# Optimization experiments

Measured on AMD Instinct MI355X. Metric: run time of the kernel, lower is better.

The kernel has to match this reference:

```python
import jax, jax.numpy as jnp
import numpy as np

THETA = 10000.0

def _rope_cache(seq_len, d_k, dtype=jnp.float32):
    # theta_k = theta ** (-(2i/d_k)), angles[n, i] = n * theta_k[i]
    inv_freq = THETA ** (-(jnp.arange(0, d_k, 2, dtype=jnp.float32) / d_k))
    pos = jnp.arange(seq_len, dtype=jnp.float32)
    ang = pos[:, None] * inv_freq[None, :]          # [S, d_k/2]
    cos = jnp.repeat(jnp.cos(ang), 2, axis=-1)      # [S, d_k]
    sin = jnp.repeat(jnp.sin(ang), 2, axis=-1)
    return cos.astype(dtype), sin.astype(dtype)

def _apply_rope(x, cos, sin):
    # x: [..., S, d_k]; rotate even/odd pairs: rot[2i] = -x[2i+1], rot[2i+1] = x[2i]
    x2 = x.reshape(x.shape[:-1] + (x.shape[-1] // 2, 2))
    rot = jnp.stack([-x2[..., 1], x2[..., 0]], axis=-1).reshape(x.shape)
    return x * cos + rot * sin

def setup_inputs() -> dict:
    key = jax.random.key(0)
    ks = jax.random.split(key, 5)
    B, S, D = 2, 2048, 1024
    H, DK = 16, 64
    scale = (2.0 / (D + DK)) ** 0.5
    x = jax.random.normal(ks[0], (B, S, D), dtype=jnp.float32)
    Wq = jax.random.normal(ks[1], (H, D, DK), dtype=jnp.float32) * scale
    Wk = jax.random.normal(ks[2], (H, D, DK), dtype=jnp.float32) * scale
    Wv = jax.random.normal(ks[3], (H, D, DK), dtype=jnp.float32) * scale
    Wo = jax.random.normal(ks[4], (D, D), dtype=jnp.float32) * (2.0 / (2 * D)) ** 0.5
    return {"x": x, "Wq": Wq, "Wk": Wk, "Wv": Wv, "Wo": Wo}

def reference(x, Wq, Wk, Wv, Wo):
    B, S, D = x.shape
    H, _, DK = Wq.shape
    cos, sin = _rope_cache(S, DK, x.dtype)          # [S, DK]
    q = jnp.einsum('bsd,hdk->bhsk', x, Wq)
    k = jnp.einsum('bsd,hdk->bhsk', x, Wk)
    v = jnp.einsum('bsd,hdk->bhsk', x, Wv)
    q = _apply_rope(q, cos, sin)
    k = _apply_rope(k, cos, sin)
    scores = jnp.einsum('bhqk,bhsk->bhqs', q, k) / jnp.sqrt(jnp.asarray(DK, x.dtype))
    causal = jnp.tril(jnp.ones((S, S), dtype=bool))
    scores = jnp.where(causal, scores, -jnp.inf)
    attn = jax.nn.softmax(scores, axis=-1)
    out = jnp.einsum('bhqs,bhsk->bhqk', attn, v)    # [B,H,S,DK]
    out = out.transpose(0, 2, 1, 3).reshape(B, S, H * DK)  # concat heads
    return jnp.einsum('bsd,do->bso', out, Wo)
```

## Files before the change

### kernel.cpp

```cpp
#include <hip/hip_runtime.h>
#include <math.h>

typedef __attribute__((ext_vector_type(8))) short bf16x8;
typedef __attribute__((ext_vector_type(4))) float f32x4;
typedef __attribute__((ext_vector_type(16))) float f32x16;
typedef __attribute__((ext_vector_type(4))) unsigned int uint32x4;
typedef __attribute__((ext_vector_type(2))) unsigned int uint32x2;
typedef unsigned short ushort_t;
typedef unsigned int uint_t;

typedef const void __attribute__((address_space(1)))* gas_ptr;
typedef void __attribute__((address_space(3)))* las_ptr;

namespace {

constexpr int S_  = 2048;
constexpr int D_  = 1024;
constexpr float CSC = 0.18033688011f;

__device__ inline ushort_t f2bf(float f) {
    uint_t u = __builtin_bit_cast(uint_t, f);
    u += 0x7FFFu + ((u >> 16) & 1u);
    return (ushort_t)(u >> 16);
}
__device__ inline uint_t cvtpk(float lo, float hi) {
    uint_t r;
    asm("v_cvt_pk_bf16_f32 %0, %1, %2" : "=v"(r) : "v"(lo), "v"(hi));
    return r;
}
__device__ inline void plswap(uint_t& d, uint_t& s) {
    uint32x2 r = __builtin_amdgcn_permlane32_swap(d, s, false, false);
    d = r[0];
    s = r[1];
}
__device__ inline float xhalf_max(float x) {
    uint_t d = __builtin_bit_cast(uint_t, x), s = d;
    plswap(d, s);
    return fmaxf(__builtin_bit_cast(float, d), __builtin_bit_cast(float, s));
}
__device__ inline float xhalf_sum(float x) {
    uint_t d = __builtin_bit_cast(uint_t, x), s = d;
    plswap(d, s);
    return __builtin_bit_cast(float, d) + __builtin_bit_cast(float, s);
}

__device__ inline void tconv_body(const float* __restrict__ src,
                                  ushort_t* __restrict__ dst,
                                  int R, int C, int r0, int c0, int tid)
{
    __shared__ float Tl[64][65];
    #pragma unroll
    for (int l = 0; l < 4; ++l) {
        int i = tid + l * 256;
        int row = i >> 4, col = (i & 15) * 4;
        float4 v = *(const float4*)(src + (size_t)(r0 + row) * C + c0 + col);
        Tl[row][col] = v.x; Tl[row][col + 1] = v.y;
        Tl[row][col + 2] = v.z; Tl[row][col + 3] = v.w;
    }
    __syncthreads();
    #pragma unroll
    for (int l = 0; l < 4; ++l) {
        int i = tid + l * 256;
        int cc = i >> 4, rr = (i & 15) * 4;
        uint_t lo = (uint_t)f2bf(Tl[rr][cc])     | ((uint_t)f2bf(Tl[rr + 1][cc]) << 16);
        uint_t hi = (uint_t)f2bf(Tl[rr + 2][cc]) | ((uint_t)f2bf(Tl[rr + 3][cc]) << 16);
        *(uint2*)(dst + (size_t)(c0 + cc) * R + r0 + rr) = make_uint2(lo, hi);
    }
}

__global__ __launch_bounds__(256)
void prep_kernel(const float* __restrict__ x,  const float* __restrict__ Wq,
                 const float* __restrict__ Wk, const float* __restrict__ Wv,
                 const float* __restrict__ Wo,
                 ushort_t* __restrict__ xb, ushort_t* __restrict__ Wt,
                 ushort_t* __restrict__ Wot, float* __restrict__ tbl)
{
    const int b = blockIdx.x, tid = threadIdx.x;
    if (b < 2048) {
        int i = b * 256 + tid;
        float4 a = ((const float4*)x)[i * 2];
        float4 c = ((const float4*)x)[i * 2 + 1];
        uint_t u0 = (uint_t)f2bf(a.x) | ((uint_t)f2bf(a.y) << 16);
        uint_t u1 = (uint_t)f2bf(a.z) | ((uint_t)f2bf(a.w) << 16);
        uint_t u2 = (uint_t)f2bf(c.x) | ((uint_t)f2bf(c.y) << 16);
        uint_t u3 = (uint_t)f2bf(c.z) | ((uint_t)f2bf(c.w) << 16);
        ((uint4*)xb)[i] = make_uint4(u0, u1, u2, u3);
    } else if (b < 2304) {
        int i = (b - 2048) * 256 + tid;
        int s = i >> 5, p = i & 31;
        float inv = powf(10000.0f, -(float)p * (1.0f / 32.0f));
        float sn, cs;
        sincosf((float)s * inv, &sn, &cs);
        ((float2*)tbl)[i] = make_float2(cs, sn);
    } else if (b < 3072) {
        int lin = b - 2304;
        int z = lin >> 4, rx = lin & 15;
        const float* src = (z < 16 ? Wq : z < 32 ? Wk : Wv) + (size_t)(z & 15) * 65536;
        tconv_body(src, Wt + (size_t)z * 65536, 1024, 64, rx * 64, 0, tid);
    } else {
        int lin = b - 3072;
        tconv_body(Wo, Wot, 1024, 1024, (lin & 15) * 64, (lin >> 4) * 64, tid);
    }
}

template<int MODE>
__global__ __launch_bounds__(256)
void gemm_kernel(const ushort_t* __restrict__ A, const ushort_t* __restrict__ Bt,
                 ushort_t* __restrict__ Qo, ushort_t* __restrict__ Ko,
                 ushort_t* __restrict__ Vto, float* __restrict__ Co,
                 const float* __restrict__ tbl, int K)
{
    constexpr int SMEM_BYTES = (MODE == 0) ? 34816 : 16384;
    __shared__ char smem[SMEM_BYTES];
    ushort_t* As = (ushort_t*)smem;
    ushort_t* Bs = As + 4096;

    const int tid  = threadIdx.x;
    const int w    = tid >> 6, lane = tid & 63;
    const int lq   = lane & 15, lk = lane >> 4;
    const int wr   = w >> 1, wc = w & 1;
    const int m0   = blockIdx.x * 128;
    const int n0   = blockIdx.y * 128;

    f32x4 acc[4][4] = {};

    for (int k0 = 0; k0 < K; k0 += 32) {
        #pragma unroll
        for (int i = 0; i < 2; ++i) {
            int c   = i * 256 + tid;
            int row = c >> 2, c4 = c & 3;
            const ushort_t* ga = A  + (size_t)(m0 + row) * K + k0 + c4 * 8;
            const ushort_t* gb = Bt + (size_t)(n0 + row) * K + k0 + c4 * 8;
            int base = (i * 256 + w * 64) * 16;
            __builtin_amdgcn_global_load_lds((gas_ptr)ga, (las_ptr)((char*)As + base), 16, 0, 0);
            __builtin_amdgcn_global_load_lds((gas_ptr)gb, (las_ptr)((char*)Bs + base), 16, 0, 0);
        }
        __syncthreads();

        bf16x8 a[4], b[4];
        #pragma unroll
        for (int m = 0; m < 4; ++m)
            a[m] = *(const bf16x8*)((const char*)As + (wr * 64 + m * 16 + lq) * 64 + lk * 16);
        #pragma unroll
        for (int n = 0; n < 4; ++n)
            b[n] = *(const bf16x8*)((const char*)Bs + (wc * 64 + n * 16 + lq) * 64 + lk * 16);
        #pragma unroll
        for (int m = 0; m < 4; ++m)
            #pragma unroll
            for (int n = 0; n < 4; ++n)
                acc[m][n] = __builtin_amdgcn_mfma_f32_16x16x32_bf16(a[m], b[n], acc[m][n], 0, 0, 0);
        __syncthreads();
    }

    if (MODE == 0) {
        const int sel = n0 >> 10;
        ushort_t* EP = (ushort_t*)smem;
        const int h0 = (n0 & 1023) >> 6;
        if (sel < 2) {
            const float sc = (sel == 0) ? CSC : 1.0f;
            #pragma unroll
            for (int m = 0; m < 4; ++m) {
                #pragma unroll
                for (int r = 0; r < 4; ++r) {
                    int lrow = wr * 64 + m * 16 + lk * 4 + r;
                    int sG = (m0 + lrow) & 2047;
                    #pragma unroll
                    for (int n = 0; n < 4; ++n) {
                        int lcol = wc * 64 + n * 16 + lq;
                        int dk = lcol & 63;
                        float v = acc[m][n][r] * sc;
                        float2 cs = *(const float2*)(tbl + ((size_t)sG * 32 + (dk >> 1)) * 2);
                        float sp = __shfl_xor(v, 1);
                        float rv = (dk & 1) ? (v * cs.x + sp * cs.y)
                                            : (v * cs.x - sp * cs.y);
                        EP[lrow * 136 + lcol] = f2bf(rv);
                    }
                }
            }
            __syncthreads();
            ushort_t* dst = (sel == 0) ? Qo : Ko;
            #pragma unroll
            for (int it = 0; it < 8; ++it) {
                int idx = it * 256 + tid;
                int row = idx >> 4, c16 = idx & 15;
                uint4 v = *(const uint4*)(EP + row * 136 + c16 * 8);
                int mg = m0 + row;
                int b_ = mg >> 11, s = mg & 2047;
                int h = h0 + (c16 >> 3);
                int dk0 = (c16 & 7) * 8;
                *(uint4*)(dst + (((size_t)b_ * 16 + h) * 2048 + s) * 64 + dk0) = v;
            }
        } else {
            #pragma unroll
            for (int m = 0; m < 4; ++m) {
                #pragma unroll
                for (int r = 0; r < 4; ++r) {
                    int lrow = wr * 64 + m * 16 + lk * 4 + r;
                    #pragma unroll
                    for (int n = 0; n < 4; ++n) {
                        int lcol = wc * 64 + n * 16 + lq;
                        EP[lcol * 136 + lrow] = f2bf(acc[m][n][r]);
                    }
                }
            }
            __syncthreads();
            #pragma unroll
            for (int it = 0; it < 8; ++it) {
                int idx = it * 256 + tid;
                int col = idx >> 4, c16 = idx & 15;
                uint4 v = *(const uint4*)(EP + col * 136 + c16 * 8);
                int h = h0 + (col >> 6);
                int dk = col & 63;
                int sb = m0 + c16 * 8;
                int b_ = sb >> 11, s = sb & 2047;
                *(uint4*)(Vto + (((size_t)b_ * 16 + h) * 64 + dk) * 2048 + s) = v;
            }
        }
    } else {
        float* EPf = (float*)smem;
        #pragma unroll
        for (int m = 0; m < 4; ++m) {
            __syncthreads();
            #pragma unroll
            for (int r = 0; r < 4; ++r) {
                int lrow = wr * 16 + lk * 4 + r;
                #pragma unroll
                for (int n = 0; n < 4; ++n) {
                    int lcol = wc * 64 + n * 16 + lq;
                    EPf[lrow * 128 + lcol] = acc[m][n][r];
                }
            }
            __syncthreads();
            #pragma unroll
            for (int it = 0; it < 4; ++it) {
                int idx = it * 256 + tid;
                int rl = idx >> 5, c32 = idx & 31;
                float4 v = *(const float4*)(EPf + rl * 128 + c32 * 4);
                int grow = m0 + (rl >> 4) * 64 + m * 16 + (rl & 15);
                *(float4*)(Co + (size_t)grow * D_ + n0 + c32 * 4) = v;
            }
        }
    }
}

__global__ __launch_bounds__(512)
void attn_kernel(const ushort_t* __restrict__ Q, const ushort_t* __restrict__ Kg,
                 const ushort_t* __restrict__ Vt, ushort_t* __restrict__ O)
{
    __shared__ ushort_t Ks[128 * 64];
    __shared__ ushort_t Vs[64 * 128];

    const int bid = blockIdx.x;
    const int c   = bid >> 8;
    const int j   = bid & 255;
    const int pg  = j >> 5;
    const int bh  = j & 31;
    const int p   = (c == 0) ? 31 - pg : (c == 1) ? pg
                  : (c == 2) ? 23 - pg : 8 + pg;

    const int tid = threadIdx.x;
    const int w = tid >> 6, lane = tid & 63;
    const int wq = w & 1, st = w >> 1;
    const int lq = lane & 31, hi = lane >> 5;
    const size_t bhBase = (size_t)bh * S_ * 64;

    const int nt   = (p >> 1) + 1;
    const int qrel = ((p & 1) << 1) + wq;

    bf16x8 qf[4];
    {
        const ushort_t* qp = Q + bhBase + (size_t)(p * 64 + wq * 32 + lq) * 64 + hi * 8;
        qf[0] = *(const bf16x8*)(qp);
        qf[1] = *(const bf16x8*)(qp + 16);
        qf[2] = *(const bf16x8*)(qp + 32);
        qf[3] = *(const bf16x8*)(qp + 48);
    }

    const int slot0 = tid, slot1 = 512 + tid;
    const int rK0 = slot0 >> 3, rK1 = slot1 >> 3;
    const int rV0 = slot0 >> 4, rV1 = slot1 >> 4;
    const ushort_t* gk0 = Kg + bhBase + (size_t)rK0 * 64 + ((slot0 & 7) ^ (rK0 & 7)) * 8;
    const ushort_t* gk1 = Kg + bhBase + (size_t)rK1 * 64 + ((slot1 & 7) ^ (rK1 & 7)) * 8;
    const ushort_t* gv0 = Vt + bhBase + (size_t)rV0 * 2048 + ((slot0 & 15) ^ (rV0 & 7)) * 8;
    const ushort_t* gv1 = Vt + bhBase + (size_t)rV1 * 2048 + ((slot1 & 15) ^ (rV1 & 7)) * 8;

    auto stage = [&](int t) {
        const size_t ko = (size_t)t * 128 * 64;
        const size_t vo = (size_t)t * 128;
        __builtin_amdgcn_global_load_lds((gas_ptr)(gk0 + ko), (las_ptr)((char*)Ks + slot0 * 16), 16, 0, 0);
        __builtin_amdgcn_global_load_lds((gas_ptr)(gk1 + ko), (las_ptr)((char*)Ks + slot1 * 16), 16, 0, 0);
        __builtin_amdgcn_global_load_lds((gas_ptr)(gv0 + vo), (las_ptr)((char*)Vs + slot0 * 16), 16, 0, 0);
        __builtin_amdgcn_global_load_lds((gas_ptr)(gv1 + vo), (las_ptr)((char*)Vs + slot1 * 16), 16, 0, 0);
    };

    float m = -1e30f, l = 0.0f;
    f32x16 oacc[2] = {};

    const int krow = st * 32 + lq;

    for (int t = 0; t < nt; ++t) {
        if (t > 0) {
            asm volatile("" ::: "memory");
            __builtin_amdgcn_s_barrier();
            asm volatile("" ::: "memory");
        }
        stage(t);
        asm volatile("s_waitcnt vmcnt(0)" ::: "memory");
        __builtin_amdgcn_s_barrier();
        asm volatile("" ::: "memory");

        const bool last = (t == nt - 1);
        if (!(last && st > qrel)) {
            f32x16 sacc = {};
            #pragma unroll
            for (int cc = 0; cc < 4; ++cc) {
                int koff = krow * 128 + ((cc * 32 + hi * 16) ^ ((krow & 7) << 4));
                bf16x8 kf = *(const bf16x8*)((const char*)Ks + koff);
                sacc = __builtin_amdgcn_mfma_f32_32x32x16_bf16(kf, qf[cc], sacc, 0, 0, 0);
            }

            if (last && st == qrel) {
                #pragma unroll
                for (int idx = 0; idx < 16; ++idx) {
                    int kvl = (idx & 3) + 8 * (idx >> 2) + 4 * hi;
                    if (kvl > lq) sacc[idx] = -1e30f;
                }
            }

            float pm = fmaxf(sacc[0], sacc[1]);
            #pragma unroll
            for (int idx = 2; idx < 16; idx += 2)
                pm = fmaxf(fmaxf(pm, sacc[idx]), sacc[idx + 1]);
            pm = xhalf_max(pm);

            if (__any(pm > m + 11.5f)) {
                float mn = fmaxf(m, pm);
                float al = exp2f(m - mn);
                m = mn;
                l *= al;
                #pragma unroll
                for (int idx = 0; idx < 16; ++idx) { oacc[0][idx] *= al; oacc[1][idx] *= al; }
            }

            float pv[16];
            #pragma unroll
            for (int idx = 0; idx < 16; ++idx) {
                float v = exp2f(sacc[idx] - m);
                pv[idx] = v;
                l += v;
            }

            #pragma unroll
            for (int c2 = 0; c2 < 2; ++c2) {
                uint_t w0 = cvtpk(pv[8 * c2 + 0], pv[8 * c2 + 1]);
                uint_t w1 = cvtpk(pv[8 * c2 + 2], pv[8 * c2 + 3]);
                uint_t w2 = cvtpk(pv[8 * c2 + 4], pv[8 * c2 + 5]);
                uint_t w3 = cvtpk(pv[8 * c2 + 6], pv[8 * c2 + 7]);
                plswap(w0, w2);
                plswap(w1, w3);
                uint32x4 pw; pw[0] = w0; pw[1] = w1; pw[2] = w2; pw[3] = w3;
                bf16x8 pb = __builtin_bit_cast(bf16x8, pw);
                #pragma unroll
                for (int d2 = 0; d2 < 2; ++d2) {
                    int vrow = d2 * 32 + lq;
                    int vslot = (st * 4 + c2 * 2 + hi) ^ (vrow & 7);
                    bf16x8 vf = *(const bf16x8*)((const char*)Vs + vrow * 256 + vslot * 16);
                    oacc[d2] = __builtin_amdgcn_mfma_f32_32x32x16_bf16(vf, pb, oacc[d2], 0, 0, 0);
                }
            }
        }
    }

    asm volatile("" ::: "memory");
    __syncthreads();

    l = xhalf_sum(l);

    float* ksf = (float*)Ks;
    float* vsf = (float*)Vs;
    const int rowi = wq * 64 + lane;
    vsf[(st * 128 + rowi) * 2 + 0] = m;
    vsf[(st * 128 + rowi) * 2 + 1] = l;
    __syncthreads();

    float msv[4], lsv[4];
    #pragma unroll
    for (int i = 0; i < 4; ++i) {
        msv[i] = vsf[(i * 128 + rowi) * 2 + 0];
        lsv[i] = vsf[(i * 128 + rowi) * 2 + 1];
    }
    float M = fmaxf(fmaxf(msv[0], msv[1]), fmaxf(msv[2], msv[3]));
    float lt = 0.0f;
    #pragma unroll
    for (int i = 0; i < 4; ++i) lt += exp2f(msv[i] - M) * lsv[i];
    const float myal = exp2f(m - M);
    const float inv  = 1.0f / lt;

    if (st == 3) {
        #pragma unroll
        for (int j2 = 0; j2 < 8; ++j2) {
            f32x4 v4;
            v4[0] = myal * oacc[j2 >> 2][(j2 & 3) * 4 + 0];
            v4[1] = myal * oacc[j2 >> 2][(j2 & 3) * 4 + 1];
            v4[2] = myal * oacc[j2 >> 2][(j2 & 3) * 4 + 2];
            v4[3] = myal * oacc[j2 >> 2][(j2 & 3) * 4 + 3];
            *(f32x4*)(ksf + rowi * 32 + ((j2 ^ (rowi & 7)) * 4)) = v4;
        }
    }
    __syncthreads();
    if (st == 2) {
        #pragma unroll
        for (int j2 = 0; j2 < 8; ++j2) {
            int soff = rowi * 32 + ((j2 ^ (rowi & 7)) * 4);
            f32x4 v4 = *(const f32x4*)(ksf + soff);
            v4[0] += myal * oacc[j2 >> 2][(j2 & 3) * 4 + 0];
            v4[1] += myal * oacc[j2 >> 2][(j2 & 3) * 4 + 1];
            v4[2] += myal * oacc[j2 >> 2][(j2 & 3) * 4 + 2];
            v4[3] += myal * oacc[j2 >> 2][(j2 & 3) * 4 + 3];
            *(f32x4*)(ksf + soff) = v4;
        }
    }
    __syncthreads();
    if (st == 1) {
        #pragma unroll
        for (int j2 = 0; j2 < 8; ++j2) {
            int soff = rowi * 32 + ((j2 ^ (rowi & 7)) * 4);
            f32x4 v4 = *(const f32x4*)(ksf + soff);
            v4[0] += myal * oacc[j2 >> 2][(j2 & 3) * 4 + 0];
            v4[1] += myal * oacc[j2 >> 2][(j2 & 3) * 4 + 1];
            v4[2] += myal * oacc[j2 >> 2][(j2 & 3) * 4 + 2];
            v4[3] += myal * oacc[j2 >> 2][(j2 & 3) * 4 + 3];
            *(f32x4*)(ksf + soff) = v4;
        }
    }
    __syncthreads();
    if (st == 0) {
        const int b_ = bh >> 4, h = bh & 15;
        const int s = p * 64 + wq * 32 + lq;
        ushort_t* ob = O + ((size_t)b_ * 2048 + s) * 1024 + h * 64;
        #pragma unroll
        for (int j2 = 0; j2 < 8; ++j2) {
            int soff = rowi * 32 + ((j2 ^ (rowi & 7)) * 4);
            f32x4 v4 = *(const f32x4*)(ksf + soff);
            int d2 = j2 >> 2, base = (j2 & 3) * 4;
            float q0 = (myal * oacc[d2][base + 0] + v4[0]) * inv;
            float q1 = (myal * oacc[d2][base + 1] + v4[1]) * inv;
            float q2 = (myal * oacc[d2][base + 2] + v4[2]) * inv;
            float q3 = (myal * oacc[d2][base + 3] + v4[3]) * inv;
            uint2 pkv;
            pkv.x = cvtpk(q0, q1);
            pkv.y = cvtpk(q2, q3);
            *(uint2*)(ob + d2 * 32 + 8 * (j2 & 3) + 4 * hi) = pkv;
        }
    }
}

}

extern "C" void kernel_launch(void* const* d_in, const int* in_sizes, int n_in,
                              void* d_out, int out_size, void* d_ws, size_t ws_size,
                              hipStream_t stream)
{
    const float* x  = (const float*)d_in[0];
    const float* Wq = (const float*)d_in[1];
    const float* Wk = (const float*)d_in[2];
    const float* Wv = (const float*)d_in[3];
    const float* Wo = (const float*)d_in[4];

    ushort_t* xb  = (ushort_t*)d_ws;
    ushort_t* Wt  = xb  + 4194304;
    ushort_t* Wot = Wt  + 3145728;
    ushort_t* Qb  = Wot + 1048576;
    ushort_t* Kb  = Qb  + 4194304;
    ushort_t* Vtb = Kb  + 4194304;
    ushort_t* Ob  = Vtb + 4194304;
    float*    tbl = (float*)(Ob + 4194304);

    prep_kernel<<<3328, 256, 0, stream>>>(x, Wq, Wk, Wv, Wo, xb, Wt, Wot, tbl);

    gemm_kernel<0><<<dim3(32, 24), 256, 0, stream>>>(xb, Wt, Qb, Kb, Vtb, nullptr, tbl, 1024);

    attn_kernel<<<1024, 512, 0, stream>>>(Qb, Kb, Vtb, Ob);

    gemm_kernel<1><<<dim3(32, 8), 256, 0, stream>>>(Ob, Wot, nullptr, nullptr, nullptr,
                                                    (float*)d_out, nullptr, 1024);
}
```

Measured before the change: 123.8 us.

## Double attention KV tile to 256 keys with two chunks per wave

```diff
diff --git a/kernel.cpp b/kernel.cpp
--- a/kernel.cpp
+++ b/kernel.cpp
@@ -247,16 +247,12 @@
 void attn_kernel(const ushort_t* __restrict__ Q, const ushort_t* __restrict__ Kg,
                  const ushort_t* __restrict__ Vt, ushort_t* __restrict__ O)
 {
-    __shared__ ushort_t Ks[128 * 64];
-    __shared__ ushort_t Vs[64 * 128];
+    __shared__ ushort_t Ks[256 * 64];
+    __shared__ ushort_t Vs[64 * 256];
 
     const int bid = blockIdx.x;
-    const int c   = bid >> 8;
-    const int j   = bid & 255;
-    const int pg  = j >> 5;
-    const int bh  = j & 31;
-    const int p   = (c == 0) ? 31 - pg : (c == 1) ? pg
-                  : (c == 2) ? 23 - pg : 8 + pg;
+    const int p  = 31 - (bid >> 5);
+    const int bh = bid & 31;
 
     const int tid = threadIdx.x;
     const int w = tid >> 6, lane = tid & 63;
@@ -264,8 +260,7 @@
     const int lq = lane & 31, hi = lane >> 5;
     const size_t bhBase = (size_t)bh * S_ * 64;
 
-    const int nt   = (p >> 1) + 1;
-    const int qrel = ((p & 1) << 1) + wq;
+    const int nt = (p >> 2) + 1;
 
     bf16x8 qf[4];
     {
@@ -276,27 +271,31 @@
         qf[3] = *(const bf16x8*)(qp + 48);
     }
 
-    const int slot0 = tid, slot1 = 512 + tid;
-    const int rK0 = slot0 >> 3, rK1 = slot1 >> 3;
-    const int rV0 = slot0 >> 4, rV1 = slot1 >> 4;
-    const ushort_t* gk0 = Kg + bhBase + (size_t)rK0 * 64 + ((slot0 & 7) ^ (rK0 & 7)) * 8;
-    const ushort_t* gk1 = Kg + bhBase + (size_t)rK1 * 64 + ((slot1 & 7) ^ (rK1 & 7)) * 8;
-    const ushort_t* gv0 = Vt + bhBase + (size_t)rV0 * 2048 + ((slot0 & 15) ^ (rV0 & 7)) * 8;
-    const ushort_t* gv1 = Vt + bhBase + (size_t)rV1 * 2048 + ((slot1 & 15) ^ (rV1 & 7)) * 8;
+    const ushort_t* gk[4];
+    const ushort_t* gv[4];
+    int lds_off[4];
+    #pragma unroll
+    for (int i = 0; i < 4; ++i) {
+        int s = tid + i * 512;
+        int rr = s >> 3, c8 = s & 7;
+        gk[i] = Kg + bhBase + (size_t)rr * 64 + (c8 ^ (rr & 7)) * 8;
+        int rv = s >> 5, c32 = s & 31;
+        gv[i] = Vt + bhBase + (size_t)rv * 2048 + (c32 ^ (rv & 7)) * 8;
+        lds_off[i] = s * 16;
+    }
 
     auto stage = [&](int t) {
-        const size_t ko = (size_t)t * 128 * 64;
-        const size_t vo = (size_t)t * 128;
-        __builtin_amdgcn_global_load_lds((gas_ptr)(gk0 + ko), (las_ptr)((char*)Ks + slot0 * 16), 16, 0, 0);
-        __builtin_amdgcn_global_load_lds((gas_ptr)(gk1 + ko), (las_ptr)((char*)Ks + slot1 * 16), 16, 0, 0);
-        __builtin_amdgcn_global_load_lds((gas_ptr)(gv0 + vo), (las_ptr)((char*)Vs + slot0 * 16), 16, 0, 0);
-        __builtin_amdgcn_global_load_lds((gas_ptr)(gv1 + vo), (las_ptr)((char*)Vs + slot1 * 16), 16, 0, 0);
+        const size_t ko = (size_t)t * 16384;
+        const size_t vo = (size_t)t * 256;
+        #pragma unroll
+        for (int i = 0; i < 4; ++i) {
+            __builtin_amdgcn_global_load_lds((gas_ptr)(gk[i] + ko), (las_ptr)((char*)Ks + lds_off[i]), 16, 0, 0);
+            __builtin_amdgcn_global_load_lds((gas_ptr)(gv[i] + vo), (las_ptr)((char*)Vs + lds_off[i]), 16, 0, 0);
+        }
     };
 
     float m = -1e30f, l = 0.0f;
     f32x16 oacc[2] = {};
-
-    const int krow = st * 32 + lq;
 
     for (int t = 0; t < nt; ++t) {
         if (t > 0) {
@@ -310,7 +309,17 @@
         asm volatile("" ::: "memory");
 
         const bool last = (t == nt - 1);
-        if (!(last && st > qrel)) {
+        #pragma unroll
+        for (int ch = 0; ch < 2; ++ch) {
+            bool tri = false;
+            if (last) {
+                int kb = t * 256 + st * 64 + ch * 32 - p * 64;
+                int qb = wq * 32;
+                if (kb > qb) continue;
+                tri = (kb == qb);
+            }
+
+            const int krow = st * 64 + ch * 32 + lq;
             f32x16 sacc = {};
             #pragma unroll
             for (int cc = 0; cc < 4; ++cc) {
@@ -319,7 +328,7 @@
                 sacc = __builtin_amdgcn_mfma_f32_32x32x16_bf16(kf, qf[cc], sacc, 0, 0, 0);
             }
 
-            if (last && st == qrel) {
+            if (tri) {
                 #pragma unroll
                 for (int idx = 0; idx < 16; ++idx) {
                     int kvl = (idx & 3) + 8 * (idx >> 2) + 4 * hi;
@@ -363,8 +372,8 @@
                 #pragma unroll
                 for (int d2 = 0; d2 < 2; ++d2) {
                     int vrow = d2 * 32 + lq;
-                    int vslot = (st * 4 + c2 * 2 + hi) ^ (vrow & 7);
-                    bf16x8 vf = *(const bf16x8*)((const char*)Vs + vrow * 256 + vslot * 16);
+                    int vslot = (st * 8 + ch * 4 + c2 * 2 + hi) ^ (vrow & 7);
+                    bf16x8 vf = *(const bf16x8*)((const char*)Vs + vrow * 512 + vslot * 16);
                     oacc[d2] = __builtin_amdgcn_mfma_f32_32x32x16_bf16(vf, pb, oacc[d2], 0, 0, 0);
                 }
             }
```

Result: no change. 122.3 us (-1.2%).
